# Optimization experiments

Measured on AMD Instinct MI355X. Metric: run time of the kernel, lower is better.

The kernel has to match this reference:

```python
import jax, jax.numpy as jnp
from jax import lax
import numpy as np

B, FRAMES, H, W = 8, 128, 64, 64
N_MFCC = 60
VID_FEAT = 196
D = VID_FEAT + N_MFCC   # COMBINE_SIZE = 256
ED = 2 * D              # mamba d_inner = 512
NST = 16                # d_state
DTR = 16                # dt_rank = ceil(D/16)
NL = 4                  # layers per direction
NC = 2                  # num_classes


def setup_inputs() -> dict:
    key = jax.random.key(0)
    ks = iter(jax.random.split(key, 64))
    def rn(shape, s=0.02):
        return jax.random.normal(next(ks), shape, jnp.float32) * s
    inp = {
        'video_input': jax.random.normal(next(ks), (B, FRAMES, 3, H, W), jnp.float32),
        'audio_input': jax.random.normal(next(ks), (B, FRAMES * N_MFCC), jnp.float32),
        'cnn_conv1_w': rn((32, 3, 3, 3), 0.1), 'cnn_conv1_b': jnp.zeros((32,), jnp.float32),
        'cnn_conv2_w': rn((64, 32, 3, 3), 0.05), 'cnn_conv2_b': jnp.zeros((64,), jnp.float32),
        'cnn_fc_w': rn((VID_FEAT, 64), 0.1), 'cnn_fc_b': jnp.zeros((VID_FEAT,), jnp.float32),
    }
    for pref in ('fwd', 'bwd'):
        inp[pref + '_norm_w'] = jnp.ones((NL, D), jnp.float32)
        inp[pref + '_in_proj_w'] = rn((NL, 2 * ED, D))
        inp[pref + '_conv_w'] = rn((NL, ED, 4), 0.1)
        inp[pref + '_conv_b'] = jnp.zeros((NL, ED), jnp.float32)
        inp[pref + '_x_proj_w'] = rn((NL, DTR + 2 * NST, ED))
        inp[pref + '_dt_w'] = rn((NL, ED, DTR), 0.1)
        inp[pref + '_dt_b'] = jnp.zeros((NL, ED), jnp.float32)
        inp[pref + '_A_log'] = jnp.tile(jnp.log(jnp.arange(1, NST + 1, dtype=jnp.float32)), (NL, ED, 1))
        inp[pref + '_D'] = jnp.ones((NL, ED), jnp.float32)
        inp[pref + '_out_proj_w'] = rn((NL, D, ED))
    inp['fc_w'] = rn((D, 2 * D)); inp['fc_b'] = jnp.zeros((D,), jnp.float32)
    inp['fc2_w'] = rn((NC, D)); inp['fc2_b'] = jnp.zeros((NC,), jnp.float32)
    return inp


def _rmsnorm(x, w, eps=1e-5):
    return x * lax.rsqrt(jnp.mean(x * x, -1, keepdims=True) + eps) * w


def _conv2d(x, w, b):
    y = lax.conv_general_dilated(x, w, (1, 1), 'SAME', dimension_numbers=('NCHW', 'OIHW', 'NCHW'))
    return y + b[None, :, None, None]


def _maxpool2(x):
    return lax.reduce_window(x, -jnp.inf, lax.max, (1, 1, 2, 2), (1, 1, 2, 2), 'VALID')


def _video_cnn(x, w1, b1, w2, b2, fw, fb):
    x = _maxpool2(jax.nn.relu(_conv2d(x, w1, b1)))
    x = _maxpool2(jax.nn.relu(_conv2d(x, w2, b2)))
    x = jnp.mean(x, (2, 3))            # global avg pool -> [B*F, 64]
    return x @ fw.T + fb               # [B*F, VID_FEAT]


def _mamba_layer(x, norm_w, in_w, conv_w, conv_b, xp_w, dt_w, dt_b, A_log, Dp, out_w):
    Bsz, L, _ = x.shape
    xn = _rmsnorm(x, norm_w)
    xz = jnp.einsum('bld,ed->ble', xn, in_w)        # [B,L,2*ED]
    xc, z = jnp.split(xz, 2, axis=-1)
    # causal depthwise conv1d, kernel 4
    xpad = jnp.pad(xc, ((0, 0), (3, 0), (0, 0)))
    xc = sum(xpad[:, k:k + L, :] * conv_w[:, k] for k in range(4)) + conv_b
    xc = jax.nn.silu(xc)
    dbc = jnp.einsum('ble,re->blr', xc, xp_w)       # [B,L,DTR+2*NST]
    dt, Bm, Cm = dbc[..., :DTR], dbc[..., DTR:DTR + NST], dbc[..., DTR + NST:]
    delta = jax.nn.softplus(jnp.einsum('blr,er->ble', dt, dt_w) + dt_b)  # [B,L,ED]
    A = -jnp.exp(A_log)                             # [ED,NST]
    dA = jnp.exp(delta[..., None] * A)              # [B,L,ED,NST]
    dBx = delta[..., None] * Bm[:, :, None, :] * xc[..., None]
    def step(h, inp):
        dA_t, dBx_t, c_t = inp
        h = dA_t * h + dBx_t
        return h, jnp.einsum('ben,bn->be', h, c_t)
    h0 = jnp.zeros((Bsz, ED, NST), x.dtype)
    _, ys = lax.scan(step, h0, (dA.transpose(1, 0, 2, 3), dBx.transpose(1, 0, 2, 3), Cm.transpose(1, 0, 2)))
    y = ys.transpose(1, 0, 2) + Dp * xc
    y = y * jax.nn.silu(z)
    return x + jnp.einsum('ble,de->bld', y, out_w)


def _mamba(x, norm_w, in_w, conv_w, conv_b, xp_w, dt_w, dt_b, A_log, Dp, out_w):
    for l in range(NL):
        x = _mamba_layer(x, norm_w[l], in_w[l], conv_w[l], conv_b[l], xp_w[l],
                         dt_w[l], dt_b[l], A_log[l], Dp[l], out_w[l])
    return x


def reference(video_input, audio_input, cnn_conv1_w, cnn_conv1_b, cnn_conv2_w, cnn_conv2_b,
              cnn_fc_w, cnn_fc_b,
              fwd_norm_w, fwd_in_proj_w, fwd_conv_w, fwd_conv_b, fwd_x_proj_w, fwd_dt_w,
              fwd_dt_b, fwd_A_log, fwd_D, fwd_out_proj_w,
              bwd_norm_w, bwd_in_proj_w, bwd_conv_w, bwd_conv_b, bwd_x_proj_w, bwd_dt_w,
              bwd_dt_b, bwd_A_log, bwd_D, bwd_out_proj_w,
              fc_w, fc_b, fc2_w, fc2_b):
    bsz, frames = video_input.shape[0], video_input.shape[1]
    xv = video_input.reshape(bsz * frames, 3, H, W)
    xv = _video_cnn(xv, cnn_conv1_w, cnn_conv1_b, cnn_conv2_w, cnn_conv2_b, cnn_fc_w, cnn_fc_b)
    xv = xv.reshape(bsz, frames, VID_FEAT)
    xa = audio_input.reshape(bsz, -1, N_MFCC)       # [B, frames, N_MFCC]
    xc = jnp.concatenate([xv, xa], axis=-1)         # [B, frames, D]
    xf = _mamba(xc, fwd_norm_w, fwd_in_proj_w, fwd_conv_w, fwd_conv_b, fwd_x_proj_w,
                fwd_dt_w, fwd_dt_b, fwd_A_log, fwd_D, fwd_out_proj_w)
    xb = _mamba(xc[:, ::-1], bwd_norm_w, bwd_in_proj_w, bwd_conv_w, bwd_conv_b, bwd_x_proj_w,
                bwd_dt_w, bwd_dt_b, bwd_A_log, bwd_D, bwd_out_proj_w)[:, ::-1]
    x_last = jnp.concatenate([xf, xb], axis=-1)[:, -1, :]   # [B, 2*D]; dropout = identity (eval)
    x = x_last @ fc_w.T + fc_b
    return x @ fc2_w.T + fc2_b
```

## Files before the change

kernel.cpp:

```cpp
#include <hip/hip_runtime.h>
#include <hip/hip_bf16.h>
#include <cstdint>
#include <cstddef>

#define BATCH 8
#define FRAMES 128
#define TOK (BATCH*FRAMES)
#define NM 60
#define VF 196
#define DD 256
#define EDIM 512
#define NSTATE 16
#define DTRANK 16
#define NLAYER 4

typedef __attribute__((ext_vector_type(8))) short short8v;
typedef __attribute__((ext_vector_type(4))) float f32x4;

__device__ __forceinline__ unsigned short f2bf(float f) {
  unsigned x = __float_as_uint(f);
  unsigned r = (x + 0x7FFFu + ((x >> 16) & 1u)) >> 16;
  return (unsigned short)r;
}
__device__ __forceinline__ float bf2f(unsigned short u) {
  return __uint_as_float((unsigned)u << 16);
}

__global__ void pack_all(const float* __restrict__ ipF, const float* __restrict__ ipR,
                         const float* __restrict__ opF, const float* __restrict__ opR,
                         const float* __restrict__ xpF, const float* __restrict__ xpR,
                         const float* __restrict__ w2, const float* __restrict__ w1,
                         unsigned short* __restrict__ Wip, unsigned short* __restrict__ Wop,
                         unsigned short* __restrict__ Wxp, unsigned short* __restrict__ Wb,
                         unsigned short* __restrict__ Wb1) {
  int id = blockIdx.x * 256 + threadIdx.x;
  if (id < 262144) {
    int dl = id >> 15, r = id & 32767;
    int ntile = r >> 9, kt = (r >> 6) & 7, lane = r & 63;
    int dir = dl >> 2, layer = dl & 3;
    const float* src = (dir ? ipR : ipF) + (size_t)layer * 1024 * 256
                       + (size_t)(ntile * 16 + (lane & 15)) * 256 + kt * 32 + (lane >> 4) * 8;
    unsigned u[4];
#pragma unroll
    for (int p = 0; p < 4; ++p)
      u[p] = (unsigned)f2bf(src[2 * p]) | ((unsigned)f2bf(src[2 * p + 1]) << 16);
    uint4 v = {u[0], u[1], u[2], u[3]};
    *(uint4*)(Wip + (size_t)id * 8) = v;
  } else if (id < 262144 + 131072) {
    int id2 = id - 262144;
    int dl = id2 >> 14, rr = id2 & 16383;
    int ntile = rr >> 10, kt = (rr >> 6) & 15, lane = rr & 63;
    int dir = dl >> 2, layer = dl & 3;
    const float* src = (dir ? opR : opF) + (size_t)layer * 256 * 512
                       + (size_t)(ntile * 16 + (lane & 15)) * 512 + kt * 32 + (lane >> 4) * 8;
    unsigned u[4];
#pragma unroll
    for (int p = 0; p < 4; ++p)
      u[p] = (unsigned)f2bf(src[2 * p]) | ((unsigned)f2bf(src[2 * p + 1]) << 16);
    uint4 v = {u[0], u[1], u[2], u[3]};
    *(uint4*)(Wop + (size_t)id2 * 8) = v;
  } else if (id < 262144 + 131072 + 24576) {
    int id3 = id - 262144 - 131072;
    int dl = id3 / 3072, rr = id3 % 3072;
    int ntile = rr >> 10, kt = (rr >> 6) & 15, lane = rr & 63;
    int dir = dl >> 2, layer = dl & 3;
    const float* src = (dir ? xpR : xpF) + (size_t)layer * 48 * 512
                       + (size_t)(ntile * 16 + (lane & 15)) * 512 + kt * 32 + (lane >> 4) * 8;
    unsigned u[4];
#pragma unroll
    for (int p = 0; p < 4; ++p)
      u[p] = (unsigned)f2bf(src[2 * p]) | ((unsigned)f2bf(src[2 * p + 1]) << 16);
    uint4 v = {u[0], u[1], u[2], u[3]};
    *(uint4*)(Wxp + (size_t)id3 * 8) = v;
  } else if (id < 417792 + 2304) {
    int id4 = id - 417792;
    int lane = id4 & 63;
    int mt = (id4 >> 6) & 3;
    int sh = id4 >> 8;
    int dy = sh / 3, dx = sh % 3;
    int oc = mt * 16 + (lane & 15);
    int ic0 = (lane >> 4) * 8;
    unsigned u[4];
#pragma unroll
    for (int p = 0; p < 4; ++p) {
      unsigned short lo = f2bf(w2[((oc * 32 + ic0 + 2 * p) * 3 + dy) * 3 + dx]);
      unsigned short hi = f2bf(w2[((oc * 32 + ic0 + 2 * p + 1) * 3 + dy) * 3 + dx]);
      u[p] = (unsigned)lo | ((unsigned)hi << 16);
    }
    uint4 v = {u[0], u[1], u[2], u[3]};
    *(uint4*)(Wb + (size_t)id4 * 8) = v;
  } else if (id < 417792 + 2304 + 128) {
    int id5 = id - 417792 - 2304;
    int mt = id5 >> 6, lane = id5 & 63;
    int oc = mt * 16 + (lane & 15);
    int ko = lane >> 4;
    unsigned u[4];
#pragma unroll
    for (int p = 0; p < 4; ++p) {
      int k0 = ko * 8 + 2 * p, k1 = k0 + 1;
      unsigned short lo = (k0 < 27) ? f2bf(w1[oc * 27 + k0]) : 0;
      unsigned short hi = (k1 < 27) ? f2bf(w1[oc * 27 + k1]) : 0;
      u[p] = (unsigned)lo | ((unsigned)hi << 16);
    }
    uint4 v = {u[0], u[1], u[2], u[3]};
    *(uint4*)(Wb1 + (size_t)id5 * 8) = v;
  }
}

#define C1RS 68
#define C1ICS 2320
__global__ __launch_bounds__(256) void conv1_mfma(
    const float* __restrict__ video, const unsigned short* __restrict__ Wb1,
    const float* __restrict__ b1, unsigned short* __restrict__ X1)
{
  __shared__ unsigned short ldsu[3 * C1ICS + 96];
  const int img = blockIdx.x >> 1, h = blockIdx.x & 1;
  const int t = threadIdx.x;
  const float* vin = video + (size_t)img * 12288;
  const int lane = t & 63, wv = t >> 6;
  const int col = lane & 15, ko = lane >> 4;

  for (int i = t; i < (3 * C1ICS + 96) / 2; i += 256) ((unsigned*)ldsu)[i] = 0;
  __syncthreads();
  for (int i = t; i < 3 * 34 * 16; i += 256) {
    int ic = i / 544, rem = i % 544, r = rem >> 4, c4 = rem & 15;
    int gr = h * 32 - 1 + r;
    if (gr < 0 || gr > 63) continue;
    float4 v = *(const float4*)(vin + ic * 4096 + gr * 64 + c4 * 4);
    unsigned lo = (unsigned)f2bf(v.x) | ((unsigned)f2bf(v.y) << 16);
    unsigned hi = (unsigned)f2bf(v.z) | ((unsigned)f2bf(v.w) << 16);
    *(uint2*)(ldsu + ic * C1ICS + r * C1RS + 4 + c4 * 4) = (uint2){lo, hi};
  }

  short8v A0 = *(const short8v*)(Wb1 + (size_t)(0 * 64 + lane) * 8);
  short8v A1 = *(const short8v*)(Wb1 + (size_t)(1 * 64 + lane) * 8);
  float bia[2][4];
#pragma unroll
  for (int mt = 0; mt < 2; ++mt)
#pragma unroll
    for (int r = 0; r < 4; ++r) bia[mt][r] = b1[mt * 16 + ko * 4 + r];

  int offs[8];
#pragma unroll
  for (int j = 0; j < 8; ++j) {
    int k = ko * 8 + j;
    int o = 0;
    if (k < 27) {
      int ic = k / 9, tap = k - ic * 9;
      int dy = tap / 3, dx = tap - dy * 3;
      o = ic * C1ICS + dy * C1RS + dx + 3;
    }
    offs[j] = o;
  }
  __syncthreads();

  f32x4 z4 = {0.f, 0.f, 0.f, 0.f};
#pragma unroll 1
  for (int rp = 0; rp < 4; ++rp) {
    const int pyl = wv * 4 + rp;
    const int y0 = 2 * pyl;
#pragma unroll
    for (int xg = 0; xg < 4; ++xg) {
      const int bse = y0 * C1RS + xg * 16 + col;
      short8v vb0, vb1;
#pragma unroll
      for (int j = 0; j < 8; ++j) {
        vb0[j] = (short)ldsu[bse + offs[j]];
        vb1[j] = (short)ldsu[bse + C1RS + offs[j]];
      }
      f32x4 c00 = __builtin_amdgcn_mfma_f32_16x16x32_bf16(A0, vb0, z4, 0, 0, 0);
      f32x4 c10 = __builtin_amdgcn_mfma_f32_16x16x32_bf16(A1, vb0, z4, 0, 0, 0);
      f32x4 c01 = __builtin_amdgcn_mfma_f32_16x16x32_bf16(A0, vb1, z4, 0, 0, 0);
      f32x4 c11 = __builtin_amdgcn_mfma_f32_16x16x32_bf16(A1, vb1, z4, 0, 0, 0);
      const int py = h * 16 + pyl;
      const int pxp = xg * 8 + (col >> 1);
#pragma unroll
      for (int mt = 0; mt < 2; ++mt) {
        f32x4 ca = mt ? c10 : c00;
        f32x4 cb = mt ? c11 : c01;
        unsigned pk[2];
#pragma unroll
        for (int r = 0; r < 4; ++r) {
          float va = fmaxf(ca[r] + bia[mt][r], 0.f);
          float vb = fmaxf(cb[r] + bia[mt][r], 0.f);
          float v = fmaxf(va, vb);
          v = fmaxf(v, __shfl_xor(v, 1, 64));
          unsigned short u = f2bf(v);
          if ((r & 1) == 0) pk[r >> 1] = (unsigned)u;
          else              pk[r >> 1] |= ((unsigned)u << 16);
        }
        if ((col & 1) == 0) {
          uint2 o = {pk[0], pk[1]};
          *(uint2*)(X1 + ((size_t)(img * 1024 + py * 32 + pxp) * 32 + mt * 16 + ko * 4)) = o;
        }
      }
    }
  }
}

#define OCT_STRIDE  (1156 * 16 + 32)
#define X_LDS_BYTES (4 * OCT_STRIDE)
__global__ __launch_bounds__(256) void conv2_k(
    const unsigned short* __restrict__ X1, const unsigned short* __restrict__ Wb,
    const float* __restrict__ b2, float* __restrict__ feat)
{
  extern __shared__ char sm[];
  float* part = (float*)(sm + X_LDS_BYTES);
  const int img = blockIdx.x, t = threadIdx.x;
  const int lane = t & 63, wv = t >> 6;
  const int kg = lane >> 4, l15 = lane & 15;

  for (int j = t; j < 1156; j += 256) {
    int r = j / 34, cc = j - r * 34;
    if (r == 0 || r == 33 || cc == 0 || cc == 33) {
      uint4 z = {0, 0, 0, 0};
#pragma unroll
      for (int oct = 0; oct < 4; ++oct)
        *(uint4*)(sm + oct * OCT_STRIDE + j * 16) = z;
    }
  }
  const uint4* src = (const uint4*)(X1 + (size_t)img * 32768);
#pragma unroll 4
  for (int i = 0; i < 16; ++i) {
    int c = i * 256 + t;
    uint4 v = src[c];
    int oct = c & 3, P = c >> 2;
    int y = P >> 5, x = P & 31;
    *(uint4*)(sm + oct * OCT_STRIDE + ((y + 1) * 34 + (x + 1)) * 16) = v;
  }
  __syncthreads();

  float bia[4][4];
#pragma unroll
  for (int mt = 0; mt < 4; ++mt)
#pragma unroll
    for (int r = 0; r < 4; ++r) bia[mt][r] = b2[mt * 16 + kg * 4 + r];

  float msum[4][4];
#pragma unroll
  for (int mt = 0; mt < 4; ++mt)
#pragma unroll
    for (int r = 0; r < 4; ++r) msum[mt][r] = 0.f;

#pragma unroll 1
  for (int pass = 0; pass < 2; ++pass) {
#pragma unroll 1
    for (int hf = 0; hf < 2; ++hf) {
#pragma unroll 1
      for (int qq = 0; qq < 2; ++qq) {
        f32x4 acc[4][2];
#pragma unroll
        for (int mt = 0; mt < 4; ++mt) {
          acc[mt][0] = (f32x4){0.f, 0.f, 0.f, 0.f};
          acc[mt][1] = (f32x4){0.f, 0.f, 0.f, 0.f};
        }
        int Pq[2];
#pragma unroll
        for (int j = 0; j < 2; ++j) {
          int qsel = qq + j * 2;
          int p = (wv * 16 + pass * 8 + hf * 4 + qsel) * 16 + l15;
          int y = p >> 5, x = p & 31;
          Pq[j] = y * 34 + x;
        }
#pragma unroll
        for (int sh = 0; sh < 9; ++sh) {
          const int dy = sh / 3, dx = sh % 3;
          const int shoff = (dy * 34 + dx) * 16;
          short8v Af[4];
#pragma unroll
          for (int mt = 0; mt < 4; ++mt)
            Af[mt] = *(const short8v*)(Wb + ((size_t)(sh * 4 + mt) * 64 + lane) * 8);
          short8v B0 = *(const short8v*)(sm + kg * OCT_STRIDE + Pq[0] * 16 + shoff);
          short8v B1 = *(const short8v*)(sm + kg * OCT_STRIDE + Pq[1] * 16 + shoff);
#pragma unroll
          for (int mt = 0; mt < 4; ++mt) {
            acc[mt][0] = __builtin_amdgcn_mfma_f32_16x16x32_bf16(Af[mt], B0, acc[mt][0], 0, 0, 0);
            acc[mt][1] = __builtin_amdgcn_mfma_f32_16x16x32_bf16(Af[mt], B1, acc[mt][1], 0, 0, 0);
          }
        }
#pragma unroll
        for (int mt = 0; mt < 4; ++mt)
#pragma unroll
          for (int r = 0; r < 4; ++r) {
            float va = fmaxf(acc[mt][0][r] + bia[mt][r], 0.f);
            float vb = fmaxf(acc[mt][1][r] + bia[mt][r], 0.f);
            float v = fmaxf(va, vb);
            v = fmaxf(v, __shfl_xor(v, 1, 64));
            msum[mt][r] += v;
          }
      }
    }
  }
#pragma unroll
  for (int mt = 0; mt < 4; ++mt)
#pragma unroll
    for (int r = 0; r < 4; ++r) {
      float v = msum[mt][r];
      v += __shfl_xor(v, 1, 64);
      v += __shfl_xor(v, 2, 64);
      v += __shfl_xor(v, 4, 64);
      v += __shfl_xor(v, 8, 64);
      if (l15 == 0) part[wv * 64 + mt * 16 + kg * 4 + r] = v * 0.5f;
    }
  __syncthreads();
  if (t < 64)
    feat[(size_t)img * 64 + t] =
        (part[t] + part[64 + t] + part[128 + t] + part[192 + t]) * (1.f / 256.f);
}

__global__ __launch_bounds__(256) void fcgemm_k(
    const float* __restrict__ A, const float* __restrict__ B,
    const float* __restrict__ bias, const float* __restrict__ audio,
    float* __restrict__ xf, float* __restrict__ xr)
{
  __shared__ float sA[16][68];
  __shared__ float sB[16][68];
  const int t = threadIdx.x;
  const int m0 = blockIdx.x * 64;
  const int n0 = blockIdx.y * 64;
  const int tx = t & 15, ty = t >> 4;
  const int lk = t & 15, lr = t >> 4;
  float acc[4][4] = {};
  for (int k0 = 0; k0 < 64; k0 += 16) {
#pragma unroll
    for (int rr = 0; rr < 4; ++rr) {
      int m = m0 + lr + rr * 16;
      sA[lk][lr + rr * 16] = A[(size_t)m * 64 + k0 + lk];
      int n = n0 + lr + rr * 16;
      sB[lk][lr + rr * 16] = (n < VF) ? B[(size_t)n * 64 + k0 + lk] : 0.f;
    }
    __syncthreads();
#pragma unroll
    for (int kk = 0; kk < 16; ++kk) {
      float a0 = sA[kk][ty*4+0], a1 = sA[kk][ty*4+1], a2 = sA[kk][ty*4+2], a3 = sA[kk][ty*4+3];
      float b0 = sB[kk][tx*4+0], b1 = sB[kk][tx*4+1], b2 = sB[kk][tx*4+2], b3 = sB[kk][tx*4+3];
      acc[0][0]=fmaf(a0,b0,acc[0][0]); acc[0][1]=fmaf(a0,b1,acc[0][1]); acc[0][2]=fmaf(a0,b2,acc[0][2]); acc[0][3]=fmaf(a0,b3,acc[0][3]);
      acc[1][0]=fmaf(a1,b0,acc[1][0]); acc[1][1]=fmaf(a1,b1,acc[1][1]); acc[1][2]=fmaf(a1,b2,acc[1][2]); acc[1][3]=fmaf(a1,b3,acc[1][3]);
      acc[2][0]=fmaf(a2,b0,acc[2][0]); acc[2][1]=fmaf(a2,b1,acc[2][1]); acc[2][2]=fmaf(a2,b2,acc[2][2]); acc[2][3]=fmaf(a2,b3,acc[2][3]);
      acc[3][0]=fmaf(a3,b0,acc[3][0]); acc[3][1]=fmaf(a3,b1,acc[3][1]); acc[3][2]=fmaf(a3,b2,acc[3][2]); acc[3][3]=fmaf(a3,b3,acc[3][3]);
    }
    __syncthreads();
  }
#pragma unroll
  for (int i = 0; i < 4; ++i) {
    int m = m0 + ty * 4 + i;
    int b = m >> 7, l = m & 127;
    int mr = (b << 7) + (127 - l);
#pragma unroll
    for (int j = 0; j < 4; ++j) {
      int n = n0 + tx * 4 + j;
      float v;
      if (n < VF)       v = acc[i][j] + bias[n];
      else              v = audio[(size_t)b * (FRAMES * NM) + l * NM + (n - VF)];
      xf[(size_t)m * DD + n] = v;
      xr[(size_t)mr * DD + n] = v;
    }
  }
}

__global__ __launch_bounds__(256) void inproj_mfma3(
    const float* __restrict__ xF, const float* __restrict__ xR,
    const float* __restrict__ nwF, const float* __restrict__ nwR,
    const unsigned short* __restrict__ Wip, int layer,
    unsigned short* __restrict__ xzF, unsigned short* __restrict__ xzR)
{
  const int dir = blockIdx.z;
  const float* x = dir ? xR : xF;
  const float* nw = dir ? nwR : nwF;
  unsigned short* xz = dir ? xzR : xzF;
  __shared__ unsigned short sa[32 * 16 * 8];
  const int t = threadIdx.x;
  const int tok0 = blockIdx.x * 16;
  {
    const int tk = t >> 4, l16 = t & 15;
    const float* row = x + (size_t)(tok0 + tk) * DD + l16 * 16;
    float v[16];
    float ss = 0.f;
#pragma unroll
    for (int i = 0; i < 4; ++i) {
      float4 f = ((const float4*)row)[i];
      v[4*i] = f.x; v[4*i+1] = f.y; v[4*i+2] = f.z; v[4*i+3] = f.w;
      ss += f.x*f.x + f.y*f.y + f.z*f.z + f.w*f.w;
    }
    ss += __shfl_xor(ss, 1, 16);
    ss += __shfl_xor(ss, 2, 16);
    ss += __shfl_xor(ss, 4, 16);
    ss += __shfl_xor(ss, 8, 16);
    float scale = rsqrtf(ss * (1.f / DD) + 1e-5f);
    const float* nwp = nw + l16 * 16;
#pragma unroll
    for (int hh = 0; hh < 2; ++hh) {
      unsigned ub[4];
#pragma unroll
      for (int p = 0; p < 4; ++p) {
        unsigned short lo = f2bf(v[hh*8 + 2*p]     * scale * nwp[hh*8 + 2*p]);
        unsigned short hi = f2bf(v[hh*8 + 2*p + 1] * scale * nwp[hh*8 + 2*p + 1]);
        ub[p] = (unsigned)lo | ((unsigned)hi << 16);
      }
      int k0 = l16 * 16 + hh * 8;
      int kt = k0 >> 5, oct = (k0 >> 3) & 3;
      uint4 w4 = {ub[0], ub[1], ub[2], ub[3]};
      *(uint4*)(sa + ((size_t)(kt * 4 + oct) * 16 + tk) * 8) = w4;
    }
  }
  __syncthreads();
  const int lane = t & 63, w = t >> 6;
  short8v af[8];
#pragma unroll
  for (int kt = 0; kt < 8; ++kt)
    af[kt] = *(const short8v*)(sa + ((size_t)(kt * 4 + (lane >> 4)) * 16 + (lane & 15)) * 8);
#pragma unroll
  for (int ns = 0; ns < 2; ++ns) {
    const int ntile = blockIdx.y * 8 + w * 2 + ns;
    const unsigned short* wb = Wip + (((size_t)(dir * 4 + layer) * 512 + ntile * 8) * 64 + lane) * 8;
    f32x4 acc = (f32x4){0.f, 0.f, 0.f, 0.f};
#pragma unroll
    for (int kt = 0; kt < 8; ++kt) {
      short8v bf = *(const short8v*)(wb + (size_t)kt * 64 * 8);
      acc = __builtin_amdgcn_mfma_f32_16x16x32_bf16(af[kt], bf, acc, 0, 0, 0);
    }
#pragma unroll
    for (int r = 0; r < 4; ++r)
      xz[(size_t)(tok0 + (lane >> 4) * 4 + r) * 1024 + ntile * 16 + (lane & 15)] = f2bf(acc[r]);
  }
}

__global__ __launch_bounds__(256) void xprojf_k(
    const unsigned short* __restrict__ xzF, const unsigned short* __restrict__ xzR,
    const float* __restrict__ cwF, const float* __restrict__ cwR,
    const float* __restrict__ cbF, const float* __restrict__ cbR,
    const unsigned short* __restrict__ Wxp, int layer,
    float* __restrict__ xcF, float* __restrict__ xcR,
    float* __restrict__ dbF, float* __restrict__ dbR)
{
  const int dir = blockIdx.z;
  const unsigned short* xz = dir ? xzR : xzF;
  const float* cw = dir ? cwR : cwF;
  const float* cb = dir ? cbR : cbF;
  float* xc = dir ? xcR : xcF;
  float* db = dir ? dbR : dbF;
  __shared__ unsigned short sa[64 * 16 * 8];
  const int t = threadIdx.x;
  const int tok0 = blockIdx.x * 16;

#pragma unroll
  for (int ii = 0; ii < 4; ++ii) {
    int idx = ii * 256 + t;
    int tk = idx >> 6, tok = tok0 + tk;
    int e0 = (idx & 63) << 3;
    int l = tok & 127;
    const unsigned short* col = xz + (size_t)tok * 1024 + e0;

    unsigned short v3[8] = {}, v2[8] = {}, v1[8] = {}, v0[8];
    if (l >= 3) *(uint4*)v3 = *(const uint4*)(col - 3 * 1024);
    if (l >= 2) *(uint4*)v2 = *(const uint4*)(col - 2 * 1024);
    if (l >= 1) *(uint4*)v1 = *(const uint4*)(col - 1 * 1024);
    *(uint4*)v0 = *(const uint4*)col;

    float cbv[8];
    *(float4*)cbv = *(const float4*)(cb + e0); *(float4*)(cbv+4) = *(const float4*)(cb + e0 + 4);

    float res[8];
#pragma unroll
    for (int j = 0; j < 8; ++j) {
      float4 cv = ((const float4*)cw)[e0 + j];
      float a = cbv[j];
      a = fmaf(cv.x, bf2f(v3[j]), a);
      a = fmaf(cv.y, bf2f(v2[j]), a);
      a = fmaf(cv.z, bf2f(v1[j]), a);
      a = fmaf(cv.w, bf2f(v0[j]), a);
      res[j] = a / (1.f + __expf(-a));
    }
    float4 r0 = {res[0], res[1], res[2], res[3]};
    float4 r1 = {res[4], res[5], res[6], res[7]};
    float* xcp = xc + (size_t)tok * EDIM + e0;
    *(float4*)xcp = r0; *(float4*)(xcp + 4) = r1;

    unsigned ub[4];
#pragma unroll
    for (int p = 0; p < 4; ++p)
      ub[p] = (unsigned)f2bf(res[2*p]) | ((unsigned)f2bf(res[2*p+1]) << 16);
    int c = (e0 >> 3) * 16 + tk;
    c ^= (c >> 4) & 15;
    uint4 w4 = {ub[0], ub[1], ub[2], ub[3]};
    *(uint4*)(sa + (size_t)c * 8) = w4;
  }
  __syncthreads();

  const int w = t >> 6, lane = t & 63;
  if (w < 3) {
    const int nt = w;
    const unsigned short* wbase = Wxp + ((size_t)(dir * 4 + layer) * 3 * 16 * 64) * 8;
    f32x4 acc = (f32x4){0.f, 0.f, 0.f, 0.f};
#pragma unroll
    for (int kt = 0; kt < 16; ++kt) {
      int c = (kt * 4 + (lane >> 4)) * 16 + (lane & 15);
      c ^= (c >> 4) & 15;
      short8v af = *(const short8v*)(sa + (size_t)c * 8);
      short8v bf = *(const short8v*)(wbase + ((size_t)(nt * 16 + kt) * 64 + lane) * 8);
      acc = __builtin_amdgcn_mfma_f32_16x16x32_bf16(af, bf, acc, 0, 0, 0);
    }
#pragma unroll
    for (int r = 0; r < 4; ++r)
      db[(size_t)(tok0 + (lane >> 4) * 4 + r) * 48 + nt * 16 + (lane & 15)] = acc[r];
  }
}

__global__ __launch_bounds__(256) void scan4_k(
    const unsigned short* __restrict__ xzF, const unsigned short* __restrict__ xzR,
    const float* __restrict__ xcF, const float* __restrict__ xcR,
    const float* __restrict__ dbF, const float* __restrict__ dbR,
    const float* __restrict__ dwF, const float* __restrict__ dwR,
    const float* __restrict__ dtbF, const float* __restrict__ dtbR,
    const float* __restrict__ AlF, const float* __restrict__ AlR,
    const float* __restrict__ DpF, const float* __restrict__ DpR,
    unsigned short* __restrict__ yoF, unsigned short* __restrict__ yoR)
{
  const int dir = blockIdx.z;
  const unsigned short* xz = dir ? xzR : xzF;
  const float* xc = dir ? xcR : xcF;
  const float* db = dir ? dbR : dbF;
  const float* dw = dir ? dwR : dwF;
  const float* dtbv = dir ? dtbR : dtbF;
  const float* Al = dir ? AlR : AlF;
  const float* Dp = dir ? DpR : DpF;
  unsigned short* yo = dir ? yoR : yoF;

  __shared__ float sdb[FRAMES * 48];
  __shared__ float sxc[FRAMES * 16];
  __shared__ float sgz[FRAMES * 16];
  __shared__ float sdl[FRAMES * 16];
  const int b = blockIdx.x >> 5;
  const int e0 = (blockIdx.x & 31) << 4;
  const int t = threadIdx.x, g = t >> 4, n = t & 15;
  const int e = e0 + g;

  const float* dbp = db + (size_t)b * FRAMES * 48;
  for (int i = t; i < FRAMES * 48 / 4; i += 256)
    ((float4*)sdb)[i] = ((const float4*)dbp)[i];
  for (int i = t; i < FRAMES * 16; i += 256) {
    int l = i >> 4, c = i & 15;
    int ee = e0 + c;
    sxc[i] = xc[(size_t)(b * FRAMES + l) * EDIM + ee];
    float zz = bf2f(xz[(size_t)(b * FRAMES + l) * 1024 + 512 + ee]);
    sgz[i] = zz / (1.f + __expf(-zz));
    const float* d = db + (size_t)(b * FRAMES + l) * 48;
    const float* w = dw + (size_t)ee * 16;
    float a = dtbv[ee];
#pragma unroll
    for (int q = 0; q < 4; ++q) {
      float4 dv = *(const float4*)(d + 4 * q);
      float4 wv = *(const float4*)(w + 4 * q);
      a = fmaf(dv.x, wv.x, a); a = fmaf(dv.y, wv.y, a);
      a = fmaf(dv.z, wv.z, a); a = fmaf(dv.w, wv.w, a);
    }
    sdl[i] = (a > 20.f) ? a : __logf(1.f + __expf(a));
  }
  float An = -expf(Al[e * NSTATE + n]);
  float Dv = Dp[e];
  float h = 0.f;
  unsigned short* yp = yo + ((size_t)((e >> 5) * 4 + ((e >> 3) & 3)) * 1024 + b * FRAMES) * 8 + (e & 7);
  __syncthreads();

#pragma unroll 1
  for (int l = 0; l < FRAMES; ++l) {
    float dlt = sdl[l * 16 + g];
    float xcv = sxc[l * 16 + g];
    float Bn = sdb[l * 48 + 16 + n];
    float Cn = sdb[l * 48 + 32 + n];
    float dA = __expf(dlt * An);
    h = fmaf(dA, h, dlt * xcv * Bn);
    float part = h * Cn;
    part += __shfl_xor(part, 1, 16);
    part += __shfl_xor(part, 2, 16);
    part += __shfl_xor(part, 4, 16);
    part += __shfl_xor(part, 8, 16);
    if (n == 0) {
      float a2 = fmaf(Dv, xcv, part);
      yp[(size_t)l * 8] = f2bf(a2 * sgz[l * 16 + g]);
    }
  }
}

__global__ __launch_bounds__(256) void outproj_mfma(
    const unsigned short* __restrict__ yoF, const unsigned short* __restrict__ yoR,
    const unsigned short* __restrict__ Wop, int layer,
    float* __restrict__ xF, float* __restrict__ xR)
{
  const int dir = blockIdx.z;
  const unsigned short* yo = dir ? yoR : yoF;
  float* xx = dir ? xR : xF;
  const int t = threadIdx.x, lane = t & 63, w = t >> 6;
  const int m0 = blockIdx.x * 16, n0 = blockIdx.y * 64;
  const int ntile = blockIdx.y * 4 + w;
  const unsigned short* wb = Wop + (((size_t)(dir * 4 + layer) * 256 + ntile * 16) * 64 + lane) * 8;
  f32x4 acc = (f32x4){0.f, 0.f, 0.f, 0.f};
#pragma unroll
  for (int kt = 0; kt < 16; ++kt) {
    short8v bf = *(const short8v*)(wb + (size_t)kt * 64 * 8);
    short8v af = *(const short8v*)(yo + ((size_t)(kt * 4 + (lane >> 4)) * 1024 + m0 + (lane & 15)) * 8);
    acc = __builtin_amdgcn_mfma_f32_16x16x32_bf16(af, bf, acc, 0, 0, 0);
  }
#pragma unroll
  for (int r = 0; r < 4; ++r) {
    size_t ci = (size_t)(m0 + (lane >> 4) * 4 + r) * DD + n0 + w * 16 + (lane & 15);
    xx[ci] += acc[r];
  }
}

__global__ __launch_bounds__(256) void head_k(
    const float* __restrict__ xf, const float* __restrict__ xr,
    const float* __restrict__ fcw, const float* __restrict__ fcb,
    const float* __restrict__ fc2w, const float* __restrict__ fc2b,
    float* __restrict__ out)
{
  int b = blockIdx.x;
  __shared__ float xl[2 * DD];
  __shared__ float h[DD];
  __shared__ float hp[4];
  int t = threadIdx.x;
  xl[t]      = xf[(size_t)(b * FRAMES + FRAMES - 1) * DD + t];
  xl[DD + t] = xr[(size_t)(b * FRAMES + 0) * DD + t];
  __syncthreads();
  float acc = fcb[t];
  for (int k = 0; k < 2 * DD; ++k) acc = fmaf(xl[k], fcw[(size_t)t * 2 * DD + k], acc);
  h[t] = acc;
  __syncthreads();
  {
    int c = t >> 7, k = t & 127;
    float p = h[k] * fc2w[c * DD + k] + h[k + 128] * fc2w[c * DD + k + 128];
#pragma unroll
    for (int off = 32; off; off >>= 1) p += __shfl_xor(p, off, 64);
    if ((t & 63) == 0) hp[t >> 6] = p;
  }
  __syncthreads();
  if (t < 2) out[b * 2 + t] = hp[2 * t] + hp[2 * t + 1] + fc2b[t];
}

extern "C" void kernel_launch(void* const* d_in, const int* in_sizes, int n_in,
                              void* d_out, int out_size, void* d_ws, size_t ws_size,
                              hipStream_t stream) {
  const float* video = (const float*)d_in[0];
  const float* audio = (const float*)d_in[1];
  const float* c1w = (const float*)d_in[2];
  const float* c1b = (const float*)d_in[3];
  const float* c2w = (const float*)d_in[4];
  const float* c2b = (const float*)d_in[5];
  const float* fcw = (const float*)d_in[6];
  const float* fcb = (const float*)d_in[7];
  const float* Wf[10]; const float* Wb_[10];
  for (int i = 0; i < 10; ++i) { Wf[i] = (const float*)d_in[8+i]; Wb_[i] = (const float*)d_in[18+i]; }
  const float* fc_w  = (const float*)d_in[28];
  const float* fc_b  = (const float*)d_in[29];
  const float* fc2_w = (const float*)d_in[30];
  const float* fc2_b = (const float*)d_in[31];
  float* out = (float*)d_out;

  float* ws   = (float*)d_ws;
  float* feat = ws;
  float* xf   = feat + 65536;
  float* xr   = xf   + 262144;
  unsigned short* xzF = (unsigned short*)(xr + 262144);
  unsigned short* xzR = (unsigned short*)(xr + 262144 + 1048576);
  float* xcF  = xr + 262144 + 2097152;
  float* xcR  = xcF  + 524288;
  float* dbF  = xcR  + 524288;
  float* dbR  = dbF  + 49152;
  unsigned short* yoF = (unsigned short*)(dbR + 49152);
  unsigned short* yoR = yoF + 524288;
  unsigned short* X1  = yoR + 524288;
  unsigned short* Wbp = X1 + 33554432;
  unsigned short* Wip = Wbp + 18432;
  unsigned short* Wop = Wip + 2097152;
  unsigned short* Wxp = Wop + 1048576;
  unsigned short* Wb1 = Wxp + 196608;

  pack_all<<<dim3(1642), 256, 0, stream>>>(Wf[1], Wb_[1], Wf[9], Wb_[9], Wf[4], Wb_[4],
                                           c2w, c1w, Wip, Wop, Wxp, Wbp, Wb1);
  conv1_mfma<<<dim3(TOK * 2), 256, 0, stream>>>(video, Wb1, c1b, X1);
  conv2_k<<<dim3(TOK), 256, (size_t)(X_LDS_BYTES + 1024), stream>>>(X1, Wbp, c2b, feat);

  fcgemm_k<<<dim3(16, 4), 256, 0, stream>>>(feat, fcw, fcb, audio, xf, xr);

  for (int l = 0; l < NLAYER; ++l) {
    const float* nwF  = Wf[0] + l*DD;              const float* nwR  = Wb_[0] + l*DD;
    const float* cwF_ = Wf[2] + l*EDIM*4;          const float* cwR_ = Wb_[2] + l*EDIM*4;
    const float* cbF_ = Wf[3] + l*EDIM;            const float* cbR_ = Wb_[3] + l*EDIM;
    const float* dwF  = Wf[5] + l*EDIM*DTRANK;     const float* dwR  = Wb_[5] + l*EDIM*DTRANK;
    const float* dtbF = Wf[6] + l*EDIM;            const float* dtbR = Wb_[6] + l*EDIM;
    const float* AlF  = Wf[7] + l*EDIM*NSTATE;     const float* AlR  = Wb_[7] + l*EDIM*NSTATE;
    const float* DpF  = Wf[8] + l*EDIM;            const float* DpR  = Wb_[8] + l*EDIM;

    inproj_mfma3<<<dim3(64, 8, 2), 256, 0, stream>>>(xf, xr, nwF, nwR, Wip, l, xzF, xzR);
    xprojf_k<<<dim3(64, 1, 2), 256, 0, stream>>>(xzF, xzR, cwF_, cwR_, cbF_, cbR_,
                                                 Wxp, l, xcF, xcR, dbF, dbR);
    scan4_k<<<dim3(256, 1, 2), 256, 0, stream>>>(xzF, xzR, xcF, xcR, dbF, dbR, dwF, dwR,
                                                 dtbF, dtbR, AlF, AlR, DpF, DpR, yoF, yoR);
    outproj_mfma<<<dim3(64, 4, 2), 256, 0, stream>>>(yoF, yoR, Wop, l, xf, xr);
  }

  head_k<<<dim3(BATCH), 256, 0, stream>>>(xf, xr, fc_w, fc_b, fc2_w, fc2_b, out);
}
```

Before: 351.5 us.

## Fuse all Mamba layer stages into one cooperative persistent kernel with grid syncs

Replaces the 16 per-layer launches (in-proj, x-proj, scan, out-proj across four layers) with a single cooperative kernel of 512 blocks that loops over layers and stages, separating stages with grid-wide syncs. This removes per-launch overhead and the gaps between kernels. It also retiles the in-proj to 4 n-tiles per wave and the out-proj to 32 rows per block. The costs are 48KB of static shared memory per block, which may limit how many blocks stay co-resident, and grid syncs that must wait for the slowest block.

```diff
diff --git a/kernel.cpp b/kernel.cpp
--- a/kernel.cpp
+++ b/kernel.cpp
@@ -1,7 +1,10 @@
 #include <hip/hip_runtime.h>
 #include <hip/hip_bf16.h>
+#include <hip/hip_cooperative_groups.h>
 #include <cstdint>
 #include <cstddef>
+
+namespace cg = cooperative_groups;
 
 #define BATCH 8
 #define FRAMES 128
@@ -13,6 +16,7 @@
 #define NSTATE 16
 #define DTRANK 16
 #define NLAYER 4
+#define CGRID 512
 
 typedef __attribute__((ext_vector_type(8))) short short8v;
 typedef __attribute__((ext_vector_type(4))) float f32x4;
@@ -358,253 +362,260 @@
   }
 }
 
-__global__ __launch_bounds__(256) void inproj_mfma3(
-    const float* __restrict__ xF, const float* __restrict__ xR,
-    const float* __restrict__ nwF, const float* __restrict__ nwR,
-    const unsigned short* __restrict__ Wip, int layer,
-    unsigned short* __restrict__ xzF, unsigned short* __restrict__ xzR)
-{
-  const int dir = blockIdx.z;
-  const float* x = dir ? xR : xF;
-  const float* nw = dir ? nwR : nwF;
-  unsigned short* xz = dir ? xzR : xzF;
-  __shared__ unsigned short sa[32 * 16 * 8];
+struct MArgs {
+  float* xf; float* xr;
+  unsigned short* xzF; unsigned short* xzR;
+  float* xcF; float* xcR;
+  float* dbF; float* dbR;
+  unsigned short* yoF; unsigned short* yoR;
+  const unsigned short* Wip; const unsigned short* Wxp; const unsigned short* Wop;
+  const float* nwF; const float* nwR;
+  const float* cwF; const float* cwR;
+  const float* cbF; const float* cbR;
+  const float* dwF; const float* dwR;
+  const float* dtbF; const float* dtbR;
+  const float* AlF; const float* AlR;
+  const float* DpF; const float* DpR;
+};
+
+__global__ __launch_bounds__(256) void mamba_all_k(MArgs a) {
+  cg::grid_group gg = cg::this_grid();
+  __shared__ char smem[49152];
   const int t = threadIdx.x;
-  const int tok0 = blockIdx.x * 16;
-  {
-    const int tk = t >> 4, l16 = t & 15;
-    const float* row = x + (size_t)(tok0 + tk) * DD + l16 * 16;
-    float v[16];
-    float ss = 0.f;
-#pragma unroll
-    for (int i = 0; i < 4; ++i) {
-      float4 f = ((const float4*)row)[i];
-      v[4*i] = f.x; v[4*i+1] = f.y; v[4*i+2] = f.z; v[4*i+3] = f.w;
-      ss += f.x*f.x + f.y*f.y + f.z*f.z + f.w*f.w;
-    }
-    ss += __shfl_xor(ss, 1, 16);
-    ss += __shfl_xor(ss, 2, 16);
-    ss += __shfl_xor(ss, 4, 16);
-    ss += __shfl_xor(ss, 8, 16);
-    float scale = rsqrtf(ss * (1.f / DD) + 1e-5f);
-    const float* nwp = nw + l16 * 16;
-#pragma unroll
-    for (int hh = 0; hh < 2; ++hh) {
-      unsigned ub[4];
-#pragma unroll
-      for (int p = 0; p < 4; ++p) {
-        unsigned short lo = f2bf(v[hh*8 + 2*p]     * scale * nwp[hh*8 + 2*p]);
-        unsigned short hi = f2bf(v[hh*8 + 2*p + 1] * scale * nwp[hh*8 + 2*p + 1]);
-        ub[p] = (unsigned)lo | ((unsigned)hi << 16);
-      }
-      int k0 = l16 * 16 + hh * 8;
-      int kt = k0 >> 5, oct = (k0 >> 3) & 3;
-      uint4 w4 = {ub[0], ub[1], ub[2], ub[3]};
-      *(uint4*)(sa + ((size_t)(kt * 4 + oct) * 16 + tk) * 8) = w4;
-    }
-  }
-  __syncthreads();
   const int lane = t & 63, w = t >> 6;
-  short8v af[8];
-#pragma unroll
-  for (int kt = 0; kt < 8; ++kt)
-    af[kt] = *(const short8v*)(sa + ((size_t)(kt * 4 + (lane >> 4)) * 16 + (lane & 15)) * 8);
-#pragma unroll
-  for (int ns = 0; ns < 2; ++ns) {
-    const int ntile = blockIdx.y * 8 + w * 2 + ns;
-    const unsigned short* wb = Wip + (((size_t)(dir * 4 + layer) * 512 + ntile * 8) * 64 + lane) * 8;
-    f32x4 acc = (f32x4){0.f, 0.f, 0.f, 0.f};
-#pragma unroll
-    for (int kt = 0; kt < 8; ++kt) {
-      short8v bf = *(const short8v*)(wb + (size_t)kt * 64 * 8);
-      acc = __builtin_amdgcn_mfma_f32_16x16x32_bf16(af[kt], bf, acc, 0, 0, 0);
-    }
-#pragma unroll
-    for (int r = 0; r < 4; ++r)
-      xz[(size_t)(tok0 + (lane >> 4) * 4 + r) * 1024 + ntile * 16 + (lane & 15)] = f2bf(acc[r]);
-  }
-}
-
-__global__ __launch_bounds__(256) void xprojf_k(
-    const unsigned short* __restrict__ xzF, const unsigned short* __restrict__ xzR,
-    const float* __restrict__ cwF, const float* __restrict__ cwR,
-    const float* __restrict__ cbF, const float* __restrict__ cbR,
-    const unsigned short* __restrict__ Wxp, int layer,
-    float* __restrict__ xcF, float* __restrict__ xcR,
-    float* __restrict__ dbF, float* __restrict__ dbR)
-{
-  const int dir = blockIdx.z;
-  const unsigned short* xz = dir ? xzR : xzF;
-  const float* cw = dir ? cwR : cwF;
-  const float* cb = dir ? cbR : cbF;
-  float* xc = dir ? xcR : xcF;
-  float* db = dir ? dbR : dbF;
-  __shared__ unsigned short sa[64 * 16 * 8];
-  const int t = threadIdx.x;
-  const int tok0 = blockIdx.x * 16;
-
-#pragma unroll
-  for (int ii = 0; ii < 4; ++ii) {
-    int idx = ii * 256 + t;
-    int tk = idx >> 6, tok = tok0 + tk;
-    int e0 = (idx & 63) << 3;
-    int l = tok & 127;
-    const unsigned short* col = xz + (size_t)tok * 1024 + e0;
-
-    unsigned short v3[8] = {}, v2[8] = {}, v1[8] = {}, v0[8];
-    if (l >= 3) *(uint4*)v3 = *(const uint4*)(col - 3 * 1024);
-    if (l >= 2) *(uint4*)v2 = *(const uint4*)(col - 2 * 1024);
-    if (l >= 1) *(uint4*)v1 = *(const uint4*)(col - 1 * 1024);
-    *(uint4*)v0 = *(const uint4*)col;
-
-    float cbv[8];
-    *(float4*)cbv = *(const float4*)(cb + e0); *(float4*)(cbv+4) = *(const float4*)(cb + e0 + 4);
-
-    float res[8];
-#pragma unroll
-    for (int j = 0; j < 8; ++j) {
-      float4 cv = ((const float4*)cw)[e0 + j];
-      float a = cbv[j];
-      a = fmaf(cv.x, bf2f(v3[j]), a);
-      a = fmaf(cv.y, bf2f(v2[j]), a);
-      a = fmaf(cv.z, bf2f(v1[j]), a);
-      a = fmaf(cv.w, bf2f(v0[j]), a);
-      res[j] = a / (1.f + __expf(-a));
-    }
-    float4 r0 = {res[0], res[1], res[2], res[3]};
-    float4 r1 = {res[4], res[5], res[6], res[7]};
-    float* xcp = xc + (size_t)tok * EDIM + e0;
-    *(float4*)xcp = r0; *(float4*)(xcp + 4) = r1;
-
-    unsigned ub[4];
-#pragma unroll
-    for (int p = 0; p < 4; ++p)
-      ub[p] = (unsigned)f2bf(res[2*p]) | ((unsigned)f2bf(res[2*p+1]) << 16);
-    int c = (e0 >> 3) * 16 + tk;
-    c ^= (c >> 4) & 15;
-    uint4 w4 = {ub[0], ub[1], ub[2], ub[3]};
-    *(uint4*)(sa + (size_t)c * 8) = w4;
-  }
-  __syncthreads();
-
-  const int w = t >> 6, lane = t & 63;
-  if (w < 3) {
-    const int nt = w;
-    const unsigned short* wbase = Wxp + ((size_t)(dir * 4 + layer) * 3 * 16 * 64) * 8;
-    f32x4 acc = (f32x4){0.f, 0.f, 0.f, 0.f};
-#pragma unroll
-    for (int kt = 0; kt < 16; ++kt) {
-      int c = (kt * 4 + (lane >> 4)) * 16 + (lane & 15);
-      c ^= (c >> 4) & 15;
-      short8v af = *(const short8v*)(sa + (size_t)c * 8);
-      short8v bf = *(const short8v*)(wbase + ((size_t)(nt * 16 + kt) * 64 + lane) * 8);
-      acc = __builtin_amdgcn_mfma_f32_16x16x32_bf16(af, bf, acc, 0, 0, 0);
-    }
-#pragma unroll
-    for (int r = 0; r < 4; ++r)
-      db[(size_t)(tok0 + (lane >> 4) * 4 + r) * 48 + nt * 16 + (lane & 15)] = acc[r];
-  }
-}
-
-__global__ __launch_bounds__(256) void scan4_k(
-    const unsigned short* __restrict__ xzF, const unsigned short* __restrict__ xzR,
-    const float* __restrict__ xcF, const float* __restrict__ xcR,
-    const float* __restrict__ dbF, const float* __restrict__ dbR,
-    const float* __restrict__ dwF, const float* __restrict__ dwR,
-    const float* __restrict__ dtbF, const float* __restrict__ dtbR,
-    const float* __restrict__ AlF, const float* __restrict__ AlR,
-    const float* __restrict__ DpF, const float* __restrict__ DpR,
-    unsigned short* __restrict__ yoF, unsigned short* __restrict__ yoR)
-{
-  const int dir = blockIdx.z;
-  const unsigned short* xz = dir ? xzR : xzF;
-  const float* xc = dir ? xcR : xcF;
-  const float* db = dir ? dbR : dbF;
-  const float* dw = dir ? dwR : dwF;
-  const float* dtbv = dir ? dtbR : dtbF;
-  const float* Al = dir ? AlR : AlF;
-  const float* Dp = dir ? DpR : DpF;
-  unsigned short* yo = dir ? yoR : yoF;
-
-  __shared__ float sdb[FRAMES * 48];
-  __shared__ float sxc[FRAMES * 16];
-  __shared__ float sgz[FRAMES * 16];
-  __shared__ float sdl[FRAMES * 16];
-  const int b = blockIdx.x >> 5;
-  const int e0 = (blockIdx.x & 31) << 4;
-  const int t = threadIdx.x, g = t >> 4, n = t & 15;
-  const int e = e0 + g;
-
-  const float* dbp = db + (size_t)b * FRAMES * 48;
-  for (int i = t; i < FRAMES * 48 / 4; i += 256)
-    ((float4*)sdb)[i] = ((const float4*)dbp)[i];
-  for (int i = t; i < FRAMES * 16; i += 256) {
-    int l = i >> 4, c = i & 15;
-    int ee = e0 + c;
-    sxc[i] = xc[(size_t)(b * FRAMES + l) * EDIM + ee];
-    float zz = bf2f(xz[(size_t)(b * FRAMES + l) * 1024 + 512 + ee]);
-    sgz[i] = zz / (1.f + __expf(-zz));
-    const float* d = db + (size_t)(b * FRAMES + l) * 48;
-    const float* w = dw + (size_t)ee * 16;
-    float a = dtbv[ee];
-#pragma unroll
-    for (int q = 0; q < 4; ++q) {
-      float4 dv = *(const float4*)(d + 4 * q);
-      float4 wv = *(const float4*)(w + 4 * q);
-      a = fmaf(dv.x, wv.x, a); a = fmaf(dv.y, wv.y, a);
-      a = fmaf(dv.z, wv.z, a); a = fmaf(dv.w, wv.w, a);
-    }
-    sdl[i] = (a > 20.f) ? a : __logf(1.f + __expf(a));
-  }
-  float An = -expf(Al[e * NSTATE + n]);
-  float Dv = Dp[e];
-  float h = 0.f;
-  unsigned short* yp = yo + ((size_t)((e >> 5) * 4 + ((e >> 3) & 3)) * 1024 + b * FRAMES) * 8 + (e & 7);
-  __syncthreads();
-
-#pragma unroll 1
-  for (int l = 0; l < FRAMES; ++l) {
-    float dlt = sdl[l * 16 + g];
-    float xcv = sxc[l * 16 + g];
-    float Bn = sdb[l * 48 + 16 + n];
-    float Cn = sdb[l * 48 + 32 + n];
-    float dA = __expf(dlt * An);
-    h = fmaf(dA, h, dlt * xcv * Bn);
-    float part = h * Cn;
-    part += __shfl_xor(part, 1, 16);
-    part += __shfl_xor(part, 2, 16);
-    part += __shfl_xor(part, 4, 16);
-    part += __shfl_xor(part, 8, 16);
-    if (n == 0) {
-      float a2 = fmaf(Dv, xcv, part);
-      yp[(size_t)l * 8] = f2bf(a2 * sgz[l * 16 + g]);
-    }
-  }
-}
-
-__global__ __launch_bounds__(256) void outproj_mfma(
-    const unsigned short* __restrict__ yoF, const unsigned short* __restrict__ yoR,
-    const unsigned short* __restrict__ Wop, int layer,
-    float* __restrict__ xF, float* __restrict__ xR)
-{
-  const int dir = blockIdx.z;
-  const unsigned short* yo = dir ? yoR : yoF;
-  float* xx = dir ? xR : xF;
-  const int t = threadIdx.x, lane = t & 63, w = t >> 6;
-  const int m0 = blockIdx.x * 16, n0 = blockIdx.y * 64;
-  const int ntile = blockIdx.y * 4 + w;
-  const unsigned short* wb = Wop + (((size_t)(dir * 4 + layer) * 256 + ntile * 16) * 64 + lane) * 8;
-  f32x4 acc = (f32x4){0.f, 0.f, 0.f, 0.f};
-#pragma unroll
-  for (int kt = 0; kt < 16; ++kt) {
-    short8v bf = *(const short8v*)(wb + (size_t)kt * 64 * 8);
-    short8v af = *(const short8v*)(yo + ((size_t)(kt * 4 + (lane >> 4)) * 1024 + m0 + (lane & 15)) * 8);
-    acc = __builtin_amdgcn_mfma_f32_16x16x32_bf16(af, bf, acc, 0, 0, 0);
-  }
-#pragma unroll
-  for (int r = 0; r < 4; ++r) {
-    size_t ci = (size_t)(m0 + (lane >> 4) * 4 + r) * DD + n0 + w * 16 + (lane & 15);
-    xx[ci] += acc[r];
+
+#pragma unroll 1
+  for (int l = 0; l < NLAYER; ++l) {
+#pragma unroll 1
+    for (int it = blockIdx.x; it < 512; it += gridDim.x) {
+      const int dir = it >> 8, r9 = it & 255;
+      const int bx = r9 & 63, by = r9 >> 6;
+      const float* x = dir ? a.xr : a.xf;
+      const float* nw = (dir ? a.nwR : a.nwF) + l * DD;
+      unsigned short* xz = dir ? a.xzR : a.xzF;
+      unsigned short* sa = (unsigned short*)smem;
+      const int tok0 = bx * 16;
+      {
+        const int tk = t >> 4, l16 = t & 15;
+        const float* row = x + (size_t)(tok0 + tk) * DD + l16 * 16;
+        float v[16];
+        float ss = 0.f;
+#pragma unroll
+        for (int i = 0; i < 4; ++i) {
+          float4 f = ((const float4*)row)[i];
+          v[4*i] = f.x; v[4*i+1] = f.y; v[4*i+2] = f.z; v[4*i+3] = f.w;
+          ss += f.x*f.x + f.y*f.y + f.z*f.z + f.w*f.w;
+        }
+        ss += __shfl_xor(ss, 1, 16);
+        ss += __shfl_xor(ss, 2, 16);
+        ss += __shfl_xor(ss, 4, 16);
+        ss += __shfl_xor(ss, 8, 16);
+        float scale = rsqrtf(ss * (1.f / DD) + 1e-5f);
+        const float* nwp = nw + l16 * 16;
+#pragma unroll
+        for (int hh = 0; hh < 2; ++hh) {
+          unsigned ub[4];
+#pragma unroll
+          for (int p = 0; p < 4; ++p) {
+            unsigned short lo = f2bf(v[hh*8 + 2*p]     * scale * nwp[hh*8 + 2*p]);
+            unsigned short hi = f2bf(v[hh*8 + 2*p + 1] * scale * nwp[hh*8 + 2*p + 1]);
+            ub[p] = (unsigned)lo | ((unsigned)hi << 16);
+          }
+          int k0 = l16 * 16 + hh * 8;
+          int kt = k0 >> 5, oct = (k0 >> 3) & 3;
+          uint4 w4 = {ub[0], ub[1], ub[2], ub[3]};
+          *(uint4*)(sa + ((size_t)(kt * 4 + oct) * 16 + tk) * 8) = w4;
+        }
+      }
+      __syncthreads();
+      short8v af[8];
+#pragma unroll
+      for (int kt = 0; kt < 8; ++kt)
+        af[kt] = *(const short8v*)(sa + ((size_t)(kt * 4 + (lane >> 4)) * 16 + (lane & 15)) * 8);
+#pragma unroll
+      for (int ns = 0; ns < 4; ++ns) {
+        const int ntile = by * 16 + w * 4 + ns;
+        const unsigned short* wb = a.Wip + (((size_t)(dir * 4 + l) * 512 + ntile * 8) * 64 + lane) * 8;
+        f32x4 acc = (f32x4){0.f, 0.f, 0.f, 0.f};
+#pragma unroll
+        for (int kt = 0; kt < 8; ++kt) {
+          short8v bf = *(const short8v*)(wb + (size_t)kt * 64 * 8);
+          acc = __builtin_amdgcn_mfma_f32_16x16x32_bf16(af[kt], bf, acc, 0, 0, 0);
+        }
+#pragma unroll
+        for (int r = 0; r < 4; ++r)
+          xz[(size_t)(tok0 + (lane >> 4) * 4 + r) * 1024 + ntile * 16 + (lane & 15)] = f2bf(acc[r]);
+      }
+      __syncthreads();
+    }
+    gg.sync();
+
+#pragma unroll 1
+    for (int it = blockIdx.x; it < 128; it += gridDim.x) {
+      const int dir = it >> 6, bx = it & 63;
+      const unsigned short* xz = dir ? a.xzR : a.xzF;
+      const float* cw = (dir ? a.cwR : a.cwF) + l * EDIM * 4;
+      const float* cb = (dir ? a.cbR : a.cbF) + l * EDIM;
+      float* xc = dir ? a.xcR : a.xcF;
+      float* db = dir ? a.dbR : a.dbF;
+      unsigned short* sa = (unsigned short*)smem;
+      const int tok0 = bx * 16;
+#pragma unroll
+      for (int ii = 0; ii < 4; ++ii) {
+        int idx = ii * 256 + t;
+        int tk = idx >> 6, tok = tok0 + tk;
+        int e0 = (idx & 63) << 3;
+        int lf = tok & 127;
+        const unsigned short* col = xz + (size_t)tok * 1024 + e0;
+        unsigned short v3[8] = {}, v2[8] = {}, v1[8] = {}, v0[8];
+        if (lf >= 3) *(uint4*)v3 = *(const uint4*)(col - 3 * 1024);
+        if (lf >= 2) *(uint4*)v2 = *(const uint4*)(col - 2 * 1024);
+        if (lf >= 1) *(uint4*)v1 = *(const uint4*)(col - 1 * 1024);
+        *(uint4*)v0 = *(const uint4*)col;
+        float cbv[8];
+        *(float4*)cbv = *(const float4*)(cb + e0); *(float4*)(cbv+4) = *(const float4*)(cb + e0 + 4);
+        float res[8];
+#pragma unroll
+        for (int j = 0; j < 8; ++j) {
+          float4 cv = ((const float4*)cw)[e0 + j];
+          float aa = cbv[j];
+          aa = fmaf(cv.x, bf2f(v3[j]), aa);
+          aa = fmaf(cv.y, bf2f(v2[j]), aa);
+          aa = fmaf(cv.z, bf2f(v1[j]), aa);
+          aa = fmaf(cv.w, bf2f(v0[j]), aa);
+          res[j] = aa / (1.f + __expf(-aa));
+        }
+        float4 r0 = {res[0], res[1], res[2], res[3]};
+        float4 r1 = {res[4], res[5], res[6], res[7]};
+        float* xcp = xc + (size_t)tok * EDIM + e0;
+        *(float4*)xcp = r0; *(float4*)(xcp + 4) = r1;
+        unsigned ub[4];
+#pragma unroll
+        for (int p = 0; p < 4; ++p)
+          ub[p] = (unsigned)f2bf(res[2*p]) | ((unsigned)f2bf(res[2*p+1]) << 16);
+        int c = (e0 >> 3) * 16 + tk;
+        c ^= (c >> 4) & 15;
+        uint4 w4 = {ub[0], ub[1], ub[2], ub[3]};
+        *(uint4*)(sa + (size_t)c * 8) = w4;
+      }
+      __syncthreads();
+      if (w < 3) {
+        const int nt = w;
+        const unsigned short* wbase = a.Wxp + ((size_t)(dir * 4 + l) * 3 * 16 * 64) * 8;
+        f32x4 acc = (f32x4){0.f, 0.f, 0.f, 0.f};
+#pragma unroll
+        for (int kt = 0; kt < 16; ++kt) {
+          int c = (kt * 4 + (lane >> 4)) * 16 + (lane & 15);
+          c ^= (c >> 4) & 15;
+          short8v af = *(const short8v*)(sa + (size_t)c * 8);
+          short8v bf = *(const short8v*)(wbase + ((size_t)(nt * 16 + kt) * 64 + lane) * 8);
+          acc = __builtin_amdgcn_mfma_f32_16x16x32_bf16(af, bf, acc, 0, 0, 0);
+        }
+#pragma unroll
+        for (int r = 0; r < 4; ++r)
+          db[(size_t)(tok0 + (lane >> 4) * 4 + r) * 48 + nt * 16 + (lane & 15)] = acc[r];
+      }
+      __syncthreads();
+    }
+    gg.sync();
+
+#pragma unroll 1
+    for (int it = blockIdx.x; it < 512; it += gridDim.x) {
+      const int dir = it >> 8, r9 = it & 255;
+      const unsigned short* xz = dir ? a.xzR : a.xzF;
+      const float* xc = dir ? a.xcR : a.xcF;
+      const float* db = dir ? a.dbR : a.dbF;
+      const float* dw = (dir ? a.dwR : a.dwF) + l * EDIM * DTRANK;
+      const float* dtbv = (dir ? a.dtbR : a.dtbF) + l * EDIM;
+      const float* Al = (dir ? a.AlR : a.AlF) + l * EDIM * NSTATE;
+      const float* Dp = (dir ? a.DpR : a.DpF) + l * EDIM;
+      unsigned short* yo = dir ? a.yoR : a.yoF;
+      float* sdb = (float*)smem;
+      float* sxc = sdb + FRAMES * 48;
+      float* sgz = sxc + FRAMES * 16;
+      float* sdl = sgz + FRAMES * 16;
+      const int b = r9 >> 5;
+      const int e0 = (r9 & 31) << 4;
+      const int g = t >> 4, n = t & 15;
+      const int e = e0 + g;
+
+      const float* dbp = db + (size_t)b * FRAMES * 48;
+      for (int i = t; i < FRAMES * 48 / 4; i += 256)
+        ((float4*)sdb)[i] = ((const float4*)dbp)[i];
+      for (int i = t; i < FRAMES * 16; i += 256) {
+        int lf = i >> 4, c = i & 15;
+        int ee = e0 + c;
+        sxc[i] = xc[(size_t)(b * FRAMES + lf) * EDIM + ee];
+        float zz = bf2f(xz[(size_t)(b * FRAMES + lf) * 1024 + 512 + ee]);
+        sgz[i] = zz / (1.f + __expf(-zz));
+        const float* d = db + (size_t)(b * FRAMES + lf) * 48;
+        const float* wp = dw + (size_t)ee * 16;
+        float aa = dtbv[ee];
+#pragma unroll
+        for (int q = 0; q < 4; ++q) {
+          float4 dv = *(const float4*)(d + 4 * q);
+          float4 wv = *(const float4*)(wp + 4 * q);
+          aa = fmaf(dv.x, wv.x, aa); aa = fmaf(dv.y, wv.y, aa);
+          aa = fmaf(dv.z, wv.z, aa); aa = fmaf(dv.w, wv.w, aa);
+        }
+        sdl[i] = (aa > 20.f) ? aa : __logf(1.f + __expf(aa));
+      }
+      float An = -expf(Al[e * NSTATE + n]);
+      float Dv = Dp[e];
+      float h = 0.f;
+      unsigned short* yp = yo + ((size_t)((e >> 5) * 4 + ((e >> 3) & 3)) * 1024 + b * FRAMES) * 8 + (e & 7);
+      __syncthreads();
+
+#pragma unroll 1
+      for (int lf = 0; lf < FRAMES; ++lf) {
+        float dlt = sdl[lf * 16 + g];
+        float xcv = sxc[lf * 16 + g];
+        float Bn = sdb[lf * 48 + 16 + n];
+        float Cn = sdb[lf * 48 + 32 + n];
+        float dA = __expf(dlt * An);
+        h = fmaf(dA, h, dlt * xcv * Bn);
+        float part = h * Cn;
+        part += __shfl_xor(part, 1, 16);
+        part += __shfl_xor(part, 2, 16);
+        part += __shfl_xor(part, 4, 16);
+        part += __shfl_xor(part, 8, 16);
+        if (n == 0) {
+          float a2 = fmaf(Dv, xcv, part);
+          yp[(size_t)lf * 8] = f2bf(a2 * sgz[lf * 16 + g]);
+        }
+      }
+      __syncthreads();
+    }
+    gg.sync();
+
+#pragma unroll 1
+    for (int it = blockIdx.x; it < 256; it += gridDim.x) {
+      const int dir = it >> 7, r9 = it & 127;
+      const int bx = r9 & 31, by = r9 >> 5;
+      const unsigned short* yo = dir ? a.yoR : a.yoF;
+      float* xx = dir ? a.xr : a.xf;
+      const int m0 = bx * 32, n0 = by * 64;
+      const int ntile = by * 4 + w;
+      const unsigned short* wb = a.Wop + (((size_t)(dir * 4 + l) * 256 + ntile * 16) * 64 + lane) * 8;
+      f32x4 acc0 = (f32x4){0.f, 0.f, 0.f, 0.f};
+      f32x4 acc1 = (f32x4){0.f, 0.f, 0.f, 0.f};
+#pragma unroll
+      for (int kt = 0; kt < 16; ++kt) {
+        short8v bf = *(const short8v*)(wb + (size_t)kt * 64 * 8);
+        short8v af0 = *(const short8v*)(yo + ((size_t)(kt * 4 + (lane >> 4)) * 1024 + m0 + (lane & 15)) * 8);
+        short8v af1 = *(const short8v*)(yo + ((size_t)(kt * 4 + (lane >> 4)) * 1024 + m0 + 16 + (lane & 15)) * 8);
+        acc0 = __builtin_amdgcn_mfma_f32_16x16x32_bf16(af0, bf, acc0, 0, 0, 0);
+        acc1 = __builtin_amdgcn_mfma_f32_16x16x32_bf16(af1, bf, acc1, 0, 0, 0);
+      }
+#pragma unroll
+      for (int r = 0; r < 4; ++r) {
+        size_t ci0 = (size_t)(m0 + (lane >> 4) * 4 + r) * DD + n0 + w * 16 + (lane & 15);
+        xx[ci0] += acc0[r];
+        size_t ci1 = (size_t)(m0 + 16 + (lane >> 4) * 4 + r) * DD + n0 + w * 16 + (lane & 15);
+        xx[ci1] += acc1[r];
+      }
+    }
+    gg.sync();
   }
 }
 
@@ -682,22 +693,23 @@
 
   fcgemm_k<<<dim3(16, 4), 256, 0, stream>>>(feat, fcw, fcb, audio, xf, xr);
 
-  for (int l = 0; l < NLAYER; ++l) {
-    const float* nwF  = Wf[0] + l*DD;              const float* nwR  = Wb_[0] + l*DD;
-    const float* cwF_ = Wf[2] + l*EDIM*4;          const float* cwR_ = Wb_[2] + l*EDIM*4;
-    const float* cbF_ = Wf[3] + l*EDIM;            const float* cbR_ = Wb_[3] + l*EDIM;
-    const float* dwF  = Wf[5] + l*EDIM*DTRANK;     const float* dwR  = Wb_[5] + l*EDIM*DTRANK;
-    const float* dtbF = Wf[6] + l*EDIM;            const float* dtbR = Wb_[6] + l*EDIM;
-    const float* AlF  = Wf[7] + l*EDIM*NSTATE;     const float* AlR  = Wb_[7] + l*EDIM*NSTATE;
-    const float* DpF  = Wf[8] + l*EDIM;            const float* DpR  = Wb_[8] + l*EDIM;
-
-    inproj_mfma3<<<dim3(64, 8, 2), 256, 0, stream>>>(xf, xr, nwF, nwR, Wip, l, xzF, xzR);
-    xprojf_k<<<dim3(64, 1, 2), 256, 0, stream>>>(xzF, xzR, cwF_, cwR_, cbF_, cbR_,
-                                                 Wxp, l, xcF, xcR, dbF, dbR);
-    scan4_k<<<dim3(256, 1, 2), 256, 0, stream>>>(xzF, xzR, xcF, xcR, dbF, dbR, dwF, dwR,
-                                                 dtbF, dtbR, AlF, AlR, DpF, DpR, yoF, yoR);
-    outproj_mfma<<<dim3(64, 4, 2), 256, 0, stream>>>(yoF, yoR, Wop, l, xf, xr);
-  }
+  MArgs ma;
+  ma.xf = xf; ma.xr = xr;
+  ma.xzF = xzF; ma.xzR = xzR;
+  ma.xcF = xcF; ma.xcR = xcR;
+  ma.dbF = dbF; ma.dbR = dbR;
+  ma.yoF = yoF; ma.yoR = yoR;
+  ma.Wip = Wip; ma.Wxp = Wxp; ma.Wop = Wop;
+  ma.nwF = Wf[0]; ma.nwR = Wb_[0];
+  ma.cwF = Wf[2]; ma.cwR = Wb_[2];
+  ma.cbF = Wf[3]; ma.cbR = Wb_[3];
+  ma.dwF = Wf[5]; ma.dwR = Wb_[5];
+  ma.dtbF = Wf[6]; ma.dtbR = Wb_[6];
+  ma.AlF = Wf[7]; ma.AlR = Wb_[7];
+  ma.DpF = Wf[8]; ma.DpR = Wb_[8];
+  void* kargs[] = { (void*)&ma };
+  hipLaunchCooperativeKernel((const void*)mamba_all_k, dim3(CGRID), dim3(256),
+                             kargs, 0, stream);
 
   head_k<<<dim3(BATCH), 256, 0, stream>>>(xf, xr, fc_w, fc_b, fc2_w, fc2_b, out);
 }
```

Measured after the change: 1.259 ms. 3.58x slower.
